# Kernel optimization log

Hardware: AMD Instinct MI355X
Metric: run time of the kernel (lower is better)

Reference implementation:

```python
import jax, jax.numpy as jnp
import numpy as np

C = 512
GROUPS = 8
EPS = 1e-5


def setup_inputs() -> dict:
    key = jax.random.key(0)
    ks = jax.random.split(key, 7)
    B, H, W = 16, 32, 32
    x = jax.random.normal(ks[0], (B, C, H, W), dtype=jnp.float32)
    gamma = jnp.ones((C,), jnp.float32)
    beta = jnp.zeros((C,), jnp.float32)
    # 1x1 convs stored as [out, in] matrices
    w_qkv = jax.random.normal(ks[1], (3 * C, C), dtype=jnp.float32) * (1.0 / np.sqrt(C))
    b_qkv = jax.random.normal(ks[2], (3 * C,), dtype=jnp.float32) * 0.02
    w_proj = jax.random.normal(ks[3], (C, C), dtype=jnp.float32) * (1.0 / np.sqrt(C))
    b_proj = jax.random.normal(ks[4], (C,), dtype=jnp.float32) * 0.02
    return {"x": x, "gamma": gamma, "beta": beta, "w_qkv": w_qkv,
            "b_qkv": b_qkv, "w_proj": w_proj, "b_proj": b_proj}


def _group_norm(x, gamma, beta):
    B, Cc, H, W = x.shape
    xg = x.reshape(B, GROUPS, Cc // GROUPS, H, W)
    mean = xg.mean(axis=(2, 3, 4), keepdims=True)
    var = xg.var(axis=(2, 3, 4), keepdims=True)
    xg = (xg - mean) * jax.lax.rsqrt(var + EPS)
    x = xg.reshape(B, Cc, H, W)
    return x * gamma[None, :, None, None] + beta[None, :, None, None]


def reference(x, gamma, beta, w_qkv, b_qkv, w_proj, b_proj):
    B, Cc, H, W = x.shape
    N = H * W
    h = _group_norm(x, gamma, beta)  # [B,C,H,W]
    hf = h.reshape(B, Cc, N)  # [B,C,N]
    # 1x1 conv == matmul over channel dim
    qkv = jnp.einsum('oc,bcn->bon', w_qkv, hf) + b_qkv[None, :, None]  # [B,3C,N]
    q, k, v = jnp.split(qkv, 3, axis=1)  # each [B,C,N]
    scale = 1.0 / jnp.sqrt(jnp.float32(Cc))
    # attn[b,i,j] = sum_c q[b,c,i] * k[b,c,j]
    attn = jnp.einsum('bci,bcj->bij', q, k) * scale  # [B,N,N]
    attn = jax.nn.softmax(attn, axis=-1)
    out = jnp.einsum('bij,bcj->bci', attn, v)  # [B,C,N]
    out = jnp.einsum('oc,bcn->bon', w_proj, out) + b_proj[None, :, None]
    return x + out.reshape(B, Cc, H, W)
```

## Files before the change

### kernel.cpp

```cpp
#include <hip/hip_runtime.h>
#include <hip/hip_bf16.h>

typedef unsigned short u16;
typedef unsigned int u32;
typedef __attribute__((ext_vector_type(8))) short short8;
typedef __attribute__((ext_vector_type(4))) float floatx4;

#define BATCH 16
#define CDIM 512
#define NSPAT 1024
#define NGROUP 8

__device__ __forceinline__ u16 f2bf(float f) {
    unsigned u = __float_as_uint(f);
    u += 0x7FFFu + ((u >> 16) & 1u);
    return (u16)(u >> 16);
}
__device__ __forceinline__ u32 f2bf2(float lo, float hi) {
    __hip_bfloat162 h = __float22bfloat162_rn(make_float2(lo, hi));
    return *(u32*)&h;
}

__device__ __forceinline__ void load_lds16(const void* g, void* l) {
    __builtin_amdgcn_global_load_lds(
        (const __attribute__((address_space(1))) unsigned int*)g,
        (__attribute__((address_space(3))) unsigned int*)l, 16, 0, 0);
}

#define SBAR0 __builtin_amdgcn_sched_barrier(0)
#define BARRIER { SBAR0; __builtin_amdgcn_s_barrier(); SBAR0; }

__global__ __launch_bounds__(256) void prep_kernel(
    const float* __restrict__ w_qkv, const float* __restrict__ w_proj,
    const float* __restrict__ b_qkv, const float* __restrict__ x,
    u16* __restrict__ wmega, u16* __restrict__ wproj_bf, u16* __restrict__ wv_t,
    float* __restrict__ stats, float* __restrict__ lsums, float* __restrict__ bpv) {
    int b = blockIdx.x;
    int tid = threadIdx.x;
    if (b < 768) {
        const float* src = (b < 512) ? w_qkv : w_proj;
        u16* dst = (b < 512) ? wmega : wproj_bf;
        int i = (b < 512 ? b : b - 512) * 256 + tid;
        float4 v = ((const float4*)src)[i];
        u32* d = (u32*)dst;
        d[i * 2] = f2bf2(v.x, v.y);
        d[i * 2 + 1] = f2bf2(v.z, v.w);
        return;
    }
    if (b < 832) {
        __shared__ u16 t[64 * 66];
        int bt = b - 768;
        int tx = bt & 7, ty = bt >> 3;
        const float* src = w_qkv + (size_t)(1024 + ty * 64) * CDIM + tx * 64;
#pragma unroll
        for (int p = 0; p < 4; ++p) {
            int r = p * 16 + (tid >> 4);
            int c4 = (tid & 15) << 2;
            float4 v = *(const float4*)(src + (size_t)r * CDIM + c4);
            u16* d = &t[r * 66 + c4];
            d[0] = f2bf(v.x); d[1] = f2bf(v.y); d[2] = f2bf(v.z); d[3] = f2bf(v.w);
        }
        __syncthreads();
        u16* dst = wv_t + (size_t)(tx * 64) * CDIM + ty * 64;
#pragma unroll
        for (int p = 0; p < 4; ++p) {
            int c = p * 16 + (tid >> 4);
            int r4 = (tid & 15) << 2;
            ushort4 o;
            o.x = t[(r4 + 0) * 66 + c];
            o.y = t[(r4 + 1) * 66 + c];
            o.z = t[(r4 + 2) * 66 + c];
            o.w = t[(r4 + 3) * 66 + c];
            *(ushort4*)(dst + (size_t)c * CDIM + r4) = o;
        }
        return;
    }
    if (b < 960) {
        __shared__ float rs[4], rss[4];
        int bg = b - 832;
        const float4* xv = (const float4*)(x + (size_t)bg * 65536);
        float s = 0.f, ss = 0.f;
        for (int i = tid; i < 16384; i += 256) {
            float4 v = xv[i];
            s += v.x + v.y + v.z + v.w;
            ss += v.x * v.x + v.y * v.y + v.z * v.z + v.w * v.w;
        }
#pragma unroll
        for (int off = 32; off; off >>= 1) { s += __shfl_down(s, off); ss += __shfl_down(ss, off); }
        int wave = tid >> 6, lane = tid & 63;
        if (lane == 0) { rs[wave] = s; rss[wave] = ss; }
        __syncthreads();
        if (tid == 0) {
            float S1 = rs[0] + rs[1] + rs[2] + rs[3];
            float S2 = rss[0] + rss[1] + rss[2] + rss[3];
            float mean = S1 * (1.f / 65536.f);
            float var = S2 * (1.f / 65536.f) - mean * mean;
            stats[bg * 2] = mean;
            stats[bg * 2 + 1] = rsqrtf(var + 1e-5f);
        }
        return;
    }
    if (b < 976) {
        ((float4*)lsums)[(b - 960) * 256 + tid] = (float4){0.f, 0.f, 0.f, 0.f};
        return;
    }
    {
        int o0 = (b - 976) * 64;
        int wave = tid >> 6, lane = tid & 63;
        const float4* bvv = (const float4*)(b_qkv + 1024);
        float4 v0 = bvv[lane * 2], v1 = bvv[lane * 2 + 1];
        for (int it = 0; it < 16; ++it) {
            int o = o0 + wave * 16 + it;
            const float4* wr = (const float4*)(w_proj + (size_t)o * CDIM);
            float4 a0 = wr[lane * 2], a1 = wr[lane * 2 + 1];
            float s = a0.x * v0.x + a0.y * v0.y + a0.z * v0.z + a0.w * v0.w
                    + a1.x * v1.x + a1.y * v1.y + a1.z * v1.z + a1.w * v1.w;
#pragma unroll
            for (int off = 32; off; off >>= 1) s += __shfl_down(s, off);
            if (lane == 0) bpv[o] = s;
        }
    }
}

__device__ __forceinline__ void stage_tile(
    const u16* __restrict__ Ab, const u16* __restrict__ Bb, int lda, int ldb,
    int m0, int n0, int k0, u16* As, u16* Bs) {
    int tid = threadIdx.x;
#pragma unroll
    for (int it = 0; it < 4; ++it) {
        int c = it * 256 + tid;
        int r = c >> 3, p = c & 7;
        int kc = p ^ (r & 7);
        load_lds16(Ab + (size_t)(m0 + r) * lda + k0 + (kc << 3), &As[c << 3]);
        load_lds16(Bb + (size_t)(n0 + r) * ldb + k0 + (kc << 3), &Bs[c << 3]);
    }
}

__device__ __forceinline__ void compute_tile(
    const u16* As, const u16* Bs, int wm, int wn, int quad, int lrow,
    floatx4 (&acc)[4][4]) {
#pragma unroll
    for (int s = 0; s < 2; ++s) {
        short8 af[4], bf[4];
#pragma unroll
        for (int i = 0; i < 4; ++i) {
            int R = wm + i * 16 + lrow;
            int p = (s * 4 + quad) ^ (R & 7);
            af[i] = *(const short8*)&As[(R << 6) + (p << 3)];
        }
#pragma unroll
        for (int j = 0; j < 4; ++j) {
            int R = wn + j * 16 + lrow;
            int p = (s * 4 + quad) ^ (R & 7);
            bf[j] = *(const short8*)&Bs[(R << 6) + (p << 3)];
        }
#pragma unroll
        for (int i = 0; i < 4; ++i)
#pragma unroll
            for (int j = 0; j < 4; ++j)
                acc[i][j] = __builtin_amdgcn_mfma_f32_16x16x32_bf16(af[i], bf[j], acc[i][j], 0, 0, 0);
    }
}

__device__ __forceinline__ void gemm_core_sb(
    const u16* __restrict__ Ab, const u16* __restrict__ Bb, int K, int lda, int ldb,
    int m0, int n0, u16* As, u16* Bs, floatx4 (&acc)[4][4]) {
    int tid = threadIdx.x;
    int lane = tid & 63, wave = tid >> 6, quad = lane >> 4, lrow = lane & 15;
    int wm = (wave >> 1) << 6, wn = (wave & 1) << 6;
    for (int k0 = 0; k0 < K; k0 += 64) {
        stage_tile(Ab, Bb, lda, ldb, m0, n0, k0, As, Bs);
        __syncthreads();
        compute_tile(As, Bs, wm, wn, quad, lrow, acc);
        __syncthreads();
    }
}

#define ACC_INIT floatx4 acc[4][4]; \
    _Pragma("unroll") for (int i = 0; i < 4; ++i) \
    _Pragma("unroll") for (int j = 0; j < 4; ++j) acc[i][j] = (floatx4){0.f, 0.f, 0.f, 0.f};

#define EPILOG_IDX int lane = threadIdx.x & 63, wave = threadIdx.x >> 6; \
    int quad = lane >> 4, lrow = lane & 15; \
    int wm = (wave >> 1) << 6, wn = (wave & 1) << 6;

__device__ __forceinline__ void issueA2(
    const u16* __restrict__ Ab, int lda, int m0, int t, int h, u16* smem) {
    int tid = threadIdx.x;
    u16* base = smem + (t & 1) * 16384 + h * 8192;
#pragma unroll
    for (int l = 0; l < 2; ++l) {
        int c = l * 512 + tid;
        int rho = c >> 3, p = c & 7;
        int kc = p ^ (rho & 7);
        int r = ((rho >> 6) << 7) | (h << 6) | (rho & 63);
        load_lds16(Ab + (size_t)(m0 + r) * lda + (t << 6) + (kc << 3), base + (c << 3));
    }
}
__device__ __forceinline__ void issueB2(
    const u16* __restrict__ Bb, int ldb, int n0, int t, int h, u16* smem) {
    int tid = threadIdx.x;
    u16* base = smem + 32768 + (t & 1) * 16384 + h * 8192;
#pragma unroll
    for (int l = 0; l < 2; ++l) {
        int c = l * 512 + tid;
        int rho = c >> 3, p = c & 7;
        int kc = p ^ (rho & 7);
        int r = ((rho >> 5) << 6) | (h << 5) | (rho & 31);
        load_lds16(Bb + (size_t)(n0 + r) * ldb + (t << 6) + (kc << 3), base + (c << 3));
    }
}

__device__ __forceinline__ void gemm256x256(
    const u16* __restrict__ Ab, const u16* __restrict__ Bb, int K, int lda, int ldb,
    int m0, int n0, u16* smem, floatx4 (&acc)[8][4]) {
    int tid = threadIdx.x;
    int lane = tid & 63, wave = tid >> 6;
    int quad = lane >> 4, lrow = lane & 15;
    int wrow = wave >> 2, wcol = wave & 3;
    int nt = K >> 6;
    issueA2(Ab, lda, m0, 0, 0, smem);
    issueA2(Ab, lda, m0, 0, 1, smem);
    issueB2(Bb, ldb, n0, 0, 0, smem);
    issueB2(Bb, ldb, n0, 0, 1, smem);
    for (int t = 0; t < nt; ++t) {
        int slot = t & 1;
        BARRIER;
        if (t + 1 < nt) {
            issueA2(Ab, lda, m0, t + 1, 0, smem);
            issueA2(Ab, lda, m0, t + 1, 1, smem);
            issueB2(Bb, ldb, n0, t + 1, 0, smem);
            issueB2(Bb, ldb, n0, t + 1, 1, smem);
            asm volatile("s_waitcnt vmcnt(8)" ::: "memory");
        } else {
            asm volatile("s_waitcnt vmcnt(0)" ::: "memory");
        }
        BARRIER;
        const u16* Ah = smem + slot * 16384;
        const u16* Bh = smem + 32768 + slot * 16384;
        short8 bf[2][4];
#pragma unroll
        for (int qn = 0; qn < 2; ++qn)
#pragma unroll
            for (int ks = 0; ks < 2; ++ks)
#pragma unroll
                for (int j = 0; j < 2; ++j) {
                    int rho = wcol * 32 + j * 16 + lrow;
                    int p = (ks * 4 + quad) ^ (lrow & 7);
                    bf[qn][ks * 2 + j] = *(const short8*)&Bh[qn * 8192 + (rho << 6) + (p << 3)];
                }
#pragma unroll
        for (int qm = 0; qm < 2; ++qm) {
            short8 af[8];
#pragma unroll
            for (int ks = 0; ks < 2; ++ks)
#pragma unroll
                for (int i = 0; i < 4; ++i) {
                    int rho = wrow * 64 + i * 16 + lrow;
                    int p = (ks * 4 + quad) ^ (lrow & 7);
                    af[ks * 4 + i] = *(const short8*)&Ah[qm * 8192 + (rho << 6) + (p << 3)];
                }
#pragma unroll
            for (int ks = 0; ks < 2; ++ks)
#pragma unroll
                for (int i = 0; i < 4; ++i)
#pragma unroll
                    for (int qn = 0; qn < 2; ++qn)
#pragma unroll
                        for (int j = 0; j < 2; ++j)
                            acc[qm * 4 + i][qn * 2 + j] = __builtin_amdgcn_mfma_f32_16x16x32_bf16(
                                af[ks * 4 + i], bf[qn][ks * 2 + j], acc[qm * 4 + i][qn * 2 + j], 0, 0, 0);
        }
    }
}

__device__ __forceinline__ void issueA4(
    const u16* __restrict__ Ab, int lda, int m0, int t, u16* smem) {
    int tid = threadIdx.x;
    u16* base = smem + (t & 1) * 16384;
#pragma unroll
    for (int l = 0; l < 4; ++l) {
        int c = l * 512 + tid;
        int rho = c >> 3, p = c & 7;
        int kc = p ^ (rho & 7);
        load_lds16(Ab + (size_t)(m0 + rho) * lda + (t << 6) + (kc << 3), base + (c << 3));
    }
}
__device__ __forceinline__ void issueB4(
    const u16* __restrict__ Bb, int ldb, int n0, int t, int h, u16* smem) {
    int tid = threadIdx.x;
    u16* base = smem + 32768 + (t & 1) * 8192 + h * 4096;
    int rho = tid >> 3, p = tid & 7;
    int kc = p ^ (rho & 7);
    int r = ((rho >> 5) << 6) | (h << 5) | (rho & 31);
    load_lds16(Bb + (size_t)(n0 + r) * ldb + (t << 6) + (kc << 3), base + (tid << 3));
}

__device__ __forceinline__ void gemm256x128(
    const u16* __restrict__ Ab, const u16* __restrict__ Bb, int K, int lda, int ldb,
    int m0, int n0, u16* smem, floatx4 (&acc)[4][4]) {
    int tid = threadIdx.x;
    int lane = tid & 63, wave = tid >> 6;
    int quad = lane >> 4, lrow = lane & 15;
    int wrow = wave >> 1, wcol = wave & 1;
    int nt = K >> 6;
    issueA4(Ab, lda, m0, 0, smem);
    issueB4(Bb, ldb, n0, 0, 0, smem);
    issueB4(Bb, ldb, n0, 0, 1, smem);
    for (int t = 0; t < nt; ++t) {
        int slot = t & 1;
        BARRIER;
        if (t + 1 < nt) {
            issueA4(Ab, lda, m0, t + 1, smem);
            issueB4(Bb, ldb, n0, t + 1, 0, smem);
            issueB4(Bb, ldb, n0, t + 1, 1, smem);
            asm volatile("s_waitcnt vmcnt(6)" ::: "memory");
        } else {
            asm volatile("s_waitcnt vmcnt(0)" ::: "memory");
        }
        BARRIER;
        const u16* Ah = smem + slot * 16384;
        const u16* Bh = smem + 32768 + slot * 8192;
        short8 bf[2][4];
#pragma unroll
        for (int qn = 0; qn < 2; ++qn)
#pragma unroll
            for (int ks = 0; ks < 2; ++ks)
#pragma unroll
                for (int j = 0; j < 2; ++j) {
                    int rho = wcol * 32 + j * 16 + lrow;
                    int p = (ks * 4 + quad) ^ (lrow & 7);
                    bf[qn][ks * 2 + j] = *(const short8*)&Bh[qn * 4096 + (rho << 6) + (p << 3)];
                }
        short8 af[8];
#pragma unroll
        for (int ks = 0; ks < 2; ++ks)
#pragma unroll
            for (int i = 0; i < 4; ++i) {
                int rho = wrow * 64 + i * 16 + lrow;
                int p = (ks * 4 + quad) ^ (lrow & 7);
                af[ks * 4 + i] = *(const short8*)&Ah[(rho << 6) + (p << 3)];
            }
#pragma unroll
        for (int ks = 0; ks < 2; ++ks)
#pragma unroll
            for (int i = 0; i < 4; ++i)
#pragma unroll
                for (int qn = 0; qn < 2; ++qn)
#pragma unroll
                    for (int j = 0; j < 2; ++j)
                        acc[i][qn * 2 + j] = __builtin_amdgcn_mfma_f32_16x16x32_bf16(
                            af[ks * 4 + i], bf[qn][ks * 2 + j], acc[i][qn * 2 + j], 0, 0, 0);
    }
}

#define ACC_INIT84 floatx4 acc[8][4]; \
    _Pragma("unroll") for (int i = 0; i < 8; ++i) \
    _Pragma("unroll") for (int j = 0; j < 4; ++j) acc[i][j] = (floatx4){0.f, 0.f, 0.f, 0.f};

#define ACC_INIT44 floatx4 acc[4][4]; \
    _Pragma("unroll") for (int i = 0; i < 4; ++i) \
    _Pragma("unroll") for (int j = 0; j < 4; ++j) acc[i][j] = (floatx4){0.f, 0.f, 0.f, 0.f};

#define TSTR 66
__global__ __launch_bounds__(256) void gn_wpv_kernel(
    const float* __restrict__ x, const float* __restrict__ gamma, const float* __restrict__ beta,
    const float* __restrict__ stats, u16* __restrict__ hT,
    const u16* __restrict__ wproj_bf, const u16* __restrict__ wv_t, u16* __restrict__ wmega) {
    __shared__ u16 smem[2 * 128 * 64];
    int tid = threadIdx.x;
    if (blockIdx.z == 16) {
        if (blockIdx.x >= 4 || blockIdx.y >= 4) return;
        int m0 = blockIdx.y << 7, n0 = blockIdx.x << 7;
        ACC_INIT;
        gemm_core_sb(wproj_bf, wv_t, CDIM, CDIM, CDIM, m0, n0, smem, smem + 128 * 64, acc);
        EPILOG_IDX;
#pragma unroll
        for (int i = 0; i < 4; ++i)
#pragma unroll
            for (int j = 0; j < 4; ++j)
#pragma unroll
                for (int r = 0; r < 4; ++r) {
                    int R = m0 + wm + i * 16 + (quad << 2) + r;
                    int Cc = n0 + wn + j * 16 + lrow;
                    wmega[(size_t)(1024 + R) * CDIM + Cc] = f2bf(acc[i][j][r]);
                }
        return;
    }
    u16* t = smem;
    int b = blockIdx.z, c0 = blockIdx.y << 6, n0 = blockIdx.x << 6;
    const float* xb = x + ((size_t)b * CDIM + c0) * NSPAT + n0;
#pragma unroll
    for (int p = 0; p < 4; ++p) {
        int cl = p * 16 + (tid >> 4);
        int nl = (tid & 15) << 2;
        int c = c0 + cl;
        int bg = b * NGROUP + (c >> 6);
        float ga = gamma[c] * stats[bg * 2 + 1];
        float be = beta[c] - stats[bg * 2] * ga;
        float4 v = *(const float4*)(xb + (size_t)cl * NSPAT + nl);
        u16* dst = &t[cl * TSTR + nl];
        dst[0] = f2bf(v.x * ga + be);
        dst[1] = f2bf(v.y * ga + be);
        dst[2] = f2bf(v.z * ga + be);
        dst[3] = f2bf(v.w * ga + be);
    }
    __syncthreads();
    u16* hb = hT + ((size_t)b * NSPAT + n0) * CDIM + c0;
#pragma unroll
    for (int p = 0; p < 4; ++p) {
        int nl = p * 16 + (tid >> 4);
        int cl4 = (tid & 15) << 2;
        ushort4 o;
        o.x = t[(cl4 + 0) * TSTR + nl];
        o.y = t[(cl4 + 1) * TSTR + nl];
        o.z = t[(cl4 + 2) * TSTR + nl];
        o.w = t[(cl4 + 3) * TSTR + nl];
        *(ushort4*)(hb + (size_t)nl * CDIM + cl4) = o;
    }
}

__global__ __launch_bounds__(512, 2) void qkv_kernel(
    const u16* __restrict__ wmega, const u16* __restrict__ hT,
    const float* __restrict__ b_qkv, const float* __restrict__ bpv,
    u16* __restrict__ qkT, u16* __restrict__ WV) {
    extern __shared__ u16 smem[];
    int z = blockIdx.x;
    int n0 = blockIdx.y << 8;
    int m0 = blockIdx.z << 8;
    const u16* Bb = hT + (size_t)z * CDIM * NSPAT;
    ACC_INIT84;
    gemm256x256(wmega, Bb, CDIM, CDIM, CDIM, m0, n0, smem, acc);
    int lane = threadIdx.x & 63, wave = threadIdx.x >> 6;
    int quad = lane >> 4, lrow = lane & 15;
    int wrow = wave >> 2, wcol = wave & 3;
    if (blockIdx.z < 4) {
        u16* qk = qkT + (size_t)z * NSPAT * NSPAT;
#pragma unroll
        for (int mf = 0; mf < 8; ++mf) {
            int R0 = m0 + wrow * 128 + mf * 16 + (quad << 2);
            float4 bv = *(const float4*)&b_qkv[R0];
#pragma unroll
            for (int nf = 0; nf < 4; ++nf) {
                int Cc = n0 + wcol * 64 + nf * 16 + lrow;
                uint2 u;
                u.x = f2bf2(acc[mf][nf][0] + bv.x, acc[mf][nf][1] + bv.y);
                u.y = f2bf2(acc[mf][nf][2] + bv.z, acc[mf][nf][3] + bv.w);
                *(uint2*)&qk[(size_t)Cc * NSPAT + R0] = u;
            }
        }
    } else {
        u16* Wp = WV + (size_t)z * CDIM * NSPAT;
#pragma unroll
        for (int mf = 0; mf < 8; ++mf) {
            int R = m0 - 1024 + wrow * 128 + mf * 16 + (quad << 2);
            float4 pv = *(const float4*)&bpv[R];
#pragma unroll
            for (int nf = 0; nf < 4; ++nf) {
                int Cc = n0 + wcol * 64 + nf * 16 + lrow;
                Wp[(size_t)(R + 0) * NSPAT + Cc] = f2bf(acc[mf][nf][0] + pv.x);
                Wp[(size_t)(R + 1) * NSPAT + Cc] = f2bf(acc[mf][nf][1] + pv.y);
                Wp[(size_t)(R + 2) * NSPAT + Cc] = f2bf(acc[mf][nf][2] + pv.z);
                Wp[(size_t)(R + 3) * NSPAT + Cc] = f2bf(acc[mf][nf][3] + pv.w);
            }
        }
    }
}

__global__ __launch_bounds__(512, 2) void scores_kernel(
    const u16* __restrict__ qkT, u16* __restrict__ P, float* __restrict__ lsums, float scale) {
    extern __shared__ u16 smem[];
    int z = blockIdx.x;
    int n0 = blockIdx.y << 8;
    int m0 = blockIdx.z << 8;
    const u16* qb = qkT + (size_t)z * NSPAT * NSPAT;
    ACC_INIT84;
    gemm256x256(qb + CDIM, qb, CDIM, NSPAT, NSPAT, m0, n0, smem, acc);
    int lane = threadIdx.x & 63, wave = threadIdx.x >> 6;
    int quad = lane >> 4, lrow = lane & 15;
    int wrow = wave >> 2, wcol = wave & 3;
    u16* Pp = P + (size_t)z * NSPAT * NSPAT;
    float* ls = lsums + (size_t)z * NSPAT;
#pragma unroll
    for (int nf = 0; nf < 4; ++nf) {
        int Ci = n0 + wcol * 64 + nf * 16 + lrow;
        float part = 0.f;
#pragma unroll
        for (int mf = 0; mf < 8; ++mf) {
            int Rj0 = m0 + wrow * 128 + mf * 16 + (quad << 2);
            float e0 = __expf(acc[mf][nf][0] * scale);
            float e1 = __expf(acc[mf][nf][1] * scale);
            float e2 = __expf(acc[mf][nf][2] * scale);
            float e3 = __expf(acc[mf][nf][3] * scale);
            part += (e0 + e1) + (e2 + e3);
            uint2 u;
            u.x = f2bf2(e0, e1);
            u.y = f2bf2(e2, e3);
            *(uint2*)&Pp[(size_t)Ci * NSPAT + Rj0] = u;
        }
        part += __shfl_xor(part, 16);
        part += __shfl_xor(part, 32);
        if (lane < 16) atomicAdd(&ls[Ci], part);
    }
}

__global__ __launch_bounds__(512, 2) void final_kernel(
    const u16* __restrict__ WV, const u16* __restrict__ P, const float* __restrict__ lsums,
    const float* __restrict__ bias, const float* __restrict__ x, float* __restrict__ out) {
    extern __shared__ u16 smem[];
    int z = blockIdx.x;
    int n0 = blockIdx.y << 7;
    int m0 = blockIdx.z << 8;
    const u16* Pb = P + (size_t)z * NSPAT * NSPAT;
    const u16* WVb = WV + (size_t)z * CDIM * NSPAT;
    ACC_INIT44;
    gemm256x128(Pb, WVb, NSPAT, NSPAT, NSPAT, m0, n0, smem, acc);
    int lane = threadIdx.x & 63, wave = threadIdx.x >> 6;
    int quad = lane >> 4, lrow = lane & 15;
    int wrow = wave >> 1, wcol = wave & 1;
    float* Op = out + (size_t)z * CDIM * NSPAT;
    const float* xr = x + (size_t)z * CDIM * NSPAT;
    const float* li = lsums + (size_t)z * NSPAT;
#pragma unroll
    for (int mf = 0; mf < 4; ++mf) {
        int Ri0 = m0 + wrow * 64 + mf * 16 + (quad << 2);
        float4 lv = *(const float4*)&li[Ri0];
        float s0 = __builtin_amdgcn_rcpf(lv.x);
        float s1 = __builtin_amdgcn_rcpf(lv.y);
        float s2 = __builtin_amdgcn_rcpf(lv.z);
        float s3 = __builtin_amdgcn_rcpf(lv.w);
#pragma unroll
        for (int nf = 0; nf < 4; ++nf) {
            int Co = n0 + wcol * 64 + nf * 16 + lrow;
            float bv = bias[Co];
            size_t off = (size_t)Co * NSPAT + Ri0;
            float4 xv = *(const float4*)&xr[off];
            float4 o;
            o.x = acc[mf][nf][0] * s0 + bv + xv.x;
            o.y = acc[mf][nf][1] * s1 + bv + xv.y;
            o.z = acc[mf][nf][2] * s2 + bv + xv.z;
            o.w = acc[mf][nf][3] * s3 + bv + xv.w;
            *(float4*)&Op[off] = o;
        }
    }
}

extern "C" void kernel_launch(void* const* d_in, const int* in_sizes, int n_in,
                              void* d_out, int out_size, void* d_ws, size_t ws_size,
                              hipStream_t stream) {
    const float* x      = (const float*)d_in[0];
    const float* gamma  = (const float*)d_in[1];
    const float* beta   = (const float*)d_in[2];
    const float* w_qkv  = (const float*)d_in[3];
    const float* b_qkv  = (const float*)d_in[4];
    const float* w_proj = (const float*)d_in[5];
    const float* b_proj = (const float*)d_in[6];
    float* out = (float*)d_out;

    const size_t CN = (size_t)CDIM * NSPAT;
    const size_t NN = (size_t)NSPAT * NSPAT;
    const float SCALE = 0.044194173824159216f;
    const int LDS_BIG = 131072;
    const int LDS_MED = 98304;

    static bool lds_attr_done = false;
    if (!lds_attr_done) {
        hipFuncSetAttribute((const void*)qkv_kernel,
                            hipFuncAttributeMaxDynamicSharedMemorySize, LDS_BIG);
        hipFuncSetAttribute((const void*)scores_kernel,
                            hipFuncAttributeMaxDynamicSharedMemorySize, LDS_BIG);
        hipFuncSetAttribute((const void*)final_kernel,
                            hipFuncAttributeMaxDynamicSharedMemorySize, LDS_MED);
        lds_attr_done = true;
    }

    char* ws = (char*)d_ws;
    float* stats   = (float*)ws;
    float* bpv     = (float*)(ws + 1024);
    u16* wmega     = (u16*)(ws + 4096);
    u16* wproj_bf  = wmega + (size_t)3 * CDIM * CDIM;
    u16* wv_t      = wproj_bf + (size_t)CDIM * CDIM;
    u16* hT        = wv_t + (size_t)CDIM * CDIM;
    u16* qkT       = hT + BATCH * CN;
    u16* WV        = qkT + BATCH * NN;
    u16* P         = WV + BATCH * CN;
    float* lsums   = (float*)(P + BATCH * NN);

    prep_kernel<<<984, 256, 0, stream>>>(
        w_qkv, w_proj, b_qkv, x, wmega, wproj_bf, wv_t, stats, lsums, bpv);

    gn_wpv_kernel<<<dim3(16, 8, 17), 256, 0, stream>>>(
        x, gamma, beta, stats, hT, wproj_bf, wv_t, wmega);

    qkv_kernel<<<dim3(BATCH, 4, 6), 512, LDS_BIG, stream>>>(
        wmega, hT, b_qkv, bpv, qkT, WV);

    scores_kernel<<<dim3(BATCH, 4, 4), 512, LDS_BIG, stream>>>(qkT, P, lsums, SCALE);

    final_kernel<<<dim3(BATCH, 4, 4), 512, LDS_MED, stream>>>(WV, P, lsums, b_proj, x, out);
}
```

Baseline: 134.8 us.

## Switch GEMMs to 256x128 tiles with triple-buffered LDS prefetch

```diff
diff --git a/kernel.cpp b/kernel.cpp
--- a/kernel.cpp
+++ b/kernel.cpp
@@ -184,100 +184,14 @@
     int quad = lane >> 4, lrow = lane & 15; \
     int wm = (wave >> 1) << 6, wn = (wave & 1) << 6;
 
-__device__ __forceinline__ void issueA2(
-    const u16* __restrict__ Ab, int lda, int m0, int t, int h, u16* smem) {
-    int tid = threadIdx.x;
-    u16* base = smem + (t & 1) * 16384 + h * 8192;
-#pragma unroll
-    for (int l = 0; l < 2; ++l) {
-        int c = l * 512 + tid;
-        int rho = c >> 3, p = c & 7;
-        int kc = p ^ (rho & 7);
-        int r = ((rho >> 6) << 7) | (h << 6) | (rho & 63);
-        load_lds16(Ab + (size_t)(m0 + r) * lda + (t << 6) + (kc << 3), base + (c << 3));
-    }
-}
-__device__ __forceinline__ void issueB2(
-    const u16* __restrict__ Bb, int ldb, int n0, int t, int h, u16* smem) {
-    int tid = threadIdx.x;
-    u16* base = smem + 32768 + (t & 1) * 16384 + h * 8192;
-#pragma unroll
-    for (int l = 0; l < 2; ++l) {
-        int c = l * 512 + tid;
-        int rho = c >> 3, p = c & 7;
-        int kc = p ^ (rho & 7);
-        int r = ((rho >> 5) << 6) | (h << 5) | (rho & 31);
-        load_lds16(Bb + (size_t)(n0 + r) * ldb + (t << 6) + (kc << 3), base + (c << 3));
-    }
-}
-
-__device__ __forceinline__ void gemm256x256(
-    const u16* __restrict__ Ab, const u16* __restrict__ Bb, int K, int lda, int ldb,
-    int m0, int n0, u16* smem, floatx4 (&acc)[8][4]) {
-    int tid = threadIdx.x;
-    int lane = tid & 63, wave = tid >> 6;
-    int quad = lane >> 4, lrow = lane & 15;
-    int wrow = wave >> 2, wcol = wave & 3;
-    int nt = K >> 6;
-    issueA2(Ab, lda, m0, 0, 0, smem);
-    issueA2(Ab, lda, m0, 0, 1, smem);
-    issueB2(Bb, ldb, n0, 0, 0, smem);
-    issueB2(Bb, ldb, n0, 0, 1, smem);
-    for (int t = 0; t < nt; ++t) {
-        int slot = t & 1;
-        BARRIER;
-        if (t + 1 < nt) {
-            issueA2(Ab, lda, m0, t + 1, 0, smem);
-            issueA2(Ab, lda, m0, t + 1, 1, smem);
-            issueB2(Bb, ldb, n0, t + 1, 0, smem);
-            issueB2(Bb, ldb, n0, t + 1, 1, smem);
-            asm volatile("s_waitcnt vmcnt(8)" ::: "memory");
-        } else {
-            asm volatile("s_waitcnt vmcnt(0)" ::: "memory");
-        }
-        BARRIER;
-        const u16* Ah = smem + slot * 16384;
-        const u16* Bh = smem + 32768 + slot * 16384;
-        short8 bf[2][4];
-#pragma unroll
-        for (int qn = 0; qn < 2; ++qn)
-#pragma unroll
-            for (int ks = 0; ks < 2; ++ks)
-#pragma unroll
-                for (int j = 0; j < 2; ++j) {
-                    int rho = wcol * 32 + j * 16 + lrow;
-                    int p = (ks * 4 + quad) ^ (lrow & 7);
-                    bf[qn][ks * 2 + j] = *(const short8*)&Bh[qn * 8192 + (rho << 6) + (p << 3)];
-                }
-#pragma unroll
-        for (int qm = 0; qm < 2; ++qm) {
-            short8 af[8];
-#pragma unroll
-            for (int ks = 0; ks < 2; ++ks)
-#pragma unroll
-                for (int i = 0; i < 4; ++i) {
-                    int rho = wrow * 64 + i * 16 + lrow;
-                    int p = (ks * 4 + quad) ^ (lrow & 7);
-                    af[ks * 4 + i] = *(const short8*)&Ah[qm * 8192 + (rho << 6) + (p << 3)];
-                }
-#pragma unroll
-            for (int ks = 0; ks < 2; ++ks)
-#pragma unroll
-                for (int i = 0; i < 4; ++i)
-#pragma unroll
-                    for (int qn = 0; qn < 2; ++qn)
-#pragma unroll
-                        for (int j = 0; j < 2; ++j)
-                            acc[qm * 4 + i][qn * 2 + j] = __builtin_amdgcn_mfma_f32_16x16x32_bf16(
-                                af[ks * 4 + i], bf[qn][ks * 2 + j], acc[qm * 4 + i][qn * 2 + j], 0, 0, 0);
-        }
-    }
-}
-
-__device__ __forceinline__ void issueA4(
-    const u16* __restrict__ Ab, int lda, int m0, int t, u16* smem) {
-    int tid = threadIdx.x;
-    u16* base = smem + (t & 1) * 16384;
+#define ASLOT 16384
+#define BSLOT 8192
+#define BBASE 49152
+
+__device__ __forceinline__ void issueA3(
+    const u16* __restrict__ Ab, int lda, int m0, int t, int slot, u16* smem) {
+    int tid = threadIdx.x;
+    u16* base = smem + slot * ASLOT;
 #pragma unroll
     for (int l = 0; l < 4; ++l) {
         int c = l * 512 + tid;
@@ -286,17 +200,20 @@
         load_lds16(Ab + (size_t)(m0 + rho) * lda + (t << 6) + (kc << 3), base + (c << 3));
     }
 }
-__device__ __forceinline__ void issueB4(
-    const u16* __restrict__ Bb, int ldb, int n0, int t, int h, u16* smem) {
-    int tid = threadIdx.x;
-    u16* base = smem + 32768 + (t & 1) * 8192 + h * 4096;
-    int rho = tid >> 3, p = tid & 7;
-    int kc = p ^ (rho & 7);
-    int r = ((rho >> 5) << 6) | (h << 5) | (rho & 31);
-    load_lds16(Bb + (size_t)(n0 + r) * ldb + (t << 6) + (kc << 3), base + (tid << 3));
-}
-
-__device__ __forceinline__ void gemm256x128(
+__device__ __forceinline__ void issueB3(
+    const u16* __restrict__ Bb, int ldb, int n0, int t, int slot, u16* smem) {
+    int tid = threadIdx.x;
+    u16* base = smem + BBASE + slot * BSLOT;
+#pragma unroll
+    for (int l = 0; l < 2; ++l) {
+        int c = l * 512 + tid;
+        int rho = c >> 3, p = c & 7;
+        int kc = p ^ (rho & 7);
+        load_lds16(Bb + (size_t)(n0 + rho) * ldb + (t << 6) + (kc << 3), base + (c << 3));
+    }
+}
+
+__device__ __forceinline__ void gemm256x128_3s(
     const u16* __restrict__ Ab, const u16* __restrict__ Bb, int K, int lda, int ldb,
     int m0, int n0, u16* smem, floatx4 (&acc)[4][4]) {
     int tid = threadIdx.x;
@@ -304,34 +221,34 @@
     int quad = lane >> 4, lrow = lane & 15;
     int wrow = wave >> 1, wcol = wave & 1;
     int nt = K >> 6;
-    issueA4(Ab, lda, m0, 0, smem);
-    issueB4(Bb, ldb, n0, 0, 0, smem);
-    issueB4(Bb, ldb, n0, 0, 1, smem);
+    issueA3(Ab, lda, m0, 0, 0, smem);
+    issueB3(Bb, ldb, n0, 0, 0, smem);
+    issueA3(Ab, lda, m0, 1, 1, smem);
+    issueB3(Bb, ldb, n0, 1, 1, smem);
+    int slot = 0, slot2 = 2;
     for (int t = 0; t < nt; ++t) {
-        int slot = t & 1;
         BARRIER;
-        if (t + 1 < nt) {
-            issueA4(Ab, lda, m0, t + 1, smem);
-            issueB4(Bb, ldb, n0, t + 1, 0, smem);
-            issueB4(Bb, ldb, n0, t + 1, 1, smem);
+        if (t + 2 < nt) {
+            issueA3(Ab, lda, m0, t + 2, slot2, smem);
+            issueB3(Bb, ldb, n0, t + 2, slot2, smem);
+            asm volatile("s_waitcnt vmcnt(12)" ::: "memory");
+        } else if (t + 1 < nt) {
             asm volatile("s_waitcnt vmcnt(6)" ::: "memory");
         } else {
             asm volatile("s_waitcnt vmcnt(0)" ::: "memory");
         }
         BARRIER;
-        const u16* Ah = smem + slot * 16384;
-        const u16* Bh = smem + 32768 + slot * 8192;
-        short8 bf[2][4];
-#pragma unroll
-        for (int qn = 0; qn < 2; ++qn)
-#pragma unroll
-            for (int ks = 0; ks < 2; ++ks)
-#pragma unroll
-                for (int j = 0; j < 2; ++j) {
-                    int rho = wcol * 32 + j * 16 + lrow;
-                    int p = (ks * 4 + quad) ^ (lrow & 7);
-                    bf[qn][ks * 2 + j] = *(const short8*)&Bh[qn * 4096 + (rho << 6) + (p << 3)];
-                }
+        const u16* Ah = smem + slot * ASLOT;
+        const u16* Bh = smem + BBASE + slot * BSLOT;
+        short8 bf[8];
+#pragma unroll
+        for (int ks = 0; ks < 2; ++ks)
+#pragma unroll
+            for (int j = 0; j < 4; ++j) {
+                int rho = wcol * 64 + j * 16 + lrow;
+                int p = (ks * 4 + quad) ^ (lrow & 7);
+                bf[ks * 4 + j] = *(const short8*)&Bh[(rho << 6) + (p << 3)];
+            }
         short8 af[8];
 #pragma unroll
         for (int ks = 0; ks < 2; ++ks)
@@ -346,21 +263,21 @@
 #pragma unroll
             for (int i = 0; i < 4; ++i)
 #pragma unroll
-                for (int qn = 0; qn < 2; ++qn)
-#pragma unroll
-                    for (int j = 0; j < 2; ++j)
-                        acc[i][qn * 2 + j] = __builtin_amdgcn_mfma_f32_16x16x32_bf16(
-                            af[ks * 4 + i], bf[qn][ks * 2 + j], acc[i][qn * 2 + j], 0, 0, 0);
-    }
-}
-
-#define ACC_INIT84 floatx4 acc[8][4]; \
-    _Pragma("unroll") for (int i = 0; i < 8; ++i) \
-    _Pragma("unroll") for (int j = 0; j < 4; ++j) acc[i][j] = (floatx4){0.f, 0.f, 0.f, 0.f};
+                for (int j = 0; j < 4; ++j)
+                    acc[i][j] = __builtin_amdgcn_mfma_f32_16x16x32_bf16(
+                        af[ks * 4 + i], bf[ks * 4 + j], acc[i][j], 0, 0, 0);
+        slot = (slot == 2) ? 0 : slot + 1;
+        slot2 = (slot2 == 2) ? 0 : slot2 + 1;
+    }
+}
 
 #define ACC_INIT44 floatx4 acc[4][4]; \
     _Pragma("unroll") for (int i = 0; i < 4; ++i) \
     _Pragma("unroll") for (int j = 0; j < 4; ++j) acc[i][j] = (floatx4){0.f, 0.f, 0.f, 0.f};
+
+#define EPILOG_IDX8 int lane = threadIdx.x & 63, wave = threadIdx.x >> 6; \
+    int quad = lane >> 4, lrow = lane & 15; \
+    int wrow = wave >> 1, wcol = wave & 1;
 
 #define TSTR 66
 __global__ __launch_bounds__(256) void gn_wpv_kernel(
@@ -420,25 +337,23 @@
     }
 }
 
-__global__ __launch_bounds__(512, 2) void qkv_kernel(
+__global__ __launch_bounds__(512, 1) void qkv_kernel(
     const u16* __restrict__ wmega, const u16* __restrict__ hT,
     const float* __restrict__ b_qkv, const float* __restrict__ bpv,
     u16* __restrict__ qkT, u16* __restrict__ WV) {
     extern __shared__ u16 smem[];
     int z = blockIdx.x;
-    int n0 = blockIdx.y << 8;
+    int n0 = blockIdx.y << 7;
     int m0 = blockIdx.z << 8;
     const u16* Bb = hT + (size_t)z * CDIM * NSPAT;
-    ACC_INIT84;
-    gemm256x256(wmega, Bb, CDIM, CDIM, CDIM, m0, n0, smem, acc);
-    int lane = threadIdx.x & 63, wave = threadIdx.x >> 6;
-    int quad = lane >> 4, lrow = lane & 15;
-    int wrow = wave >> 2, wcol = wave & 3;
+    ACC_INIT44;
+    gemm256x128_3s(wmega, Bb, CDIM, CDIM, CDIM, m0, n0, smem, acc);
+    EPILOG_IDX8;
     if (blockIdx.z < 4) {
         u16* qk = qkT + (size_t)z * NSPAT * NSPAT;
 #pragma unroll
-        for (int mf = 0; mf < 8; ++mf) {
-            int R0 = m0 + wrow * 128 + mf * 16 + (quad << 2);
+        for (int mf = 0; mf < 4; ++mf) {
+            int R0 = m0 + wrow * 64 + mf * 16 + (quad << 2);
             float4 bv = *(const float4*)&b_qkv[R0];
 #pragma unroll
             for (int nf = 0; nf < 4; ++nf) {
@@ -452,8 +367,8 @@
     } else {
         u16* Wp = WV + (size_t)z * CDIM * NSPAT;
 #pragma unroll
-        for (int mf = 0; mf < 8; ++mf) {
-            int R = m0 - 1024 + wrow * 128 + mf * 16 + (quad << 2);
+        for (int mf = 0; mf < 4; ++mf) {
+            int R = m0 - 1024 + wrow * 64 + mf * 16 + (quad << 2);
             float4 pv = *(const float4*)&bpv[R];
 #pragma unroll
             for (int nf = 0; nf < 4; ++nf) {
@@ -467,18 +382,16 @@
     }
 }
 
-__global__ __launch_bounds__(512, 2) void scores_kernel(
+__global__ __launch_bounds__(512, 1) void scores_kernel(
     const u16* __restrict__ qkT, u16* __restrict__ P, float* __restrict__ lsums, float scale) {
     extern __shared__ u16 smem[];
     int z = blockIdx.x;
-    int n0 = blockIdx.y << 8;
+    int n0 = blockIdx.y << 7;
     int m0 = blockIdx.z << 8;
     const u16* qb = qkT + (size_t)z * NSPAT * NSPAT;
-    ACC_INIT84;
-    gemm256x256(qb + CDIM, qb, CDIM, NSPAT, NSPAT, m0, n0, smem, acc);
-    int lane = threadIdx.x & 63, wave = threadIdx.x >> 6;
-    int quad = lane >> 4, lrow = lane & 15;
-    int wrow = wave >> 2, wcol = wave & 3;
+    ACC_INIT44;
+    gemm256x128_3s(qb + CDIM, qb, CDIM, NSPAT, NSPAT, m0, n0, smem, acc);
+    EPILOG_IDX8;
     u16* Pp = P + (size_t)z * NSPAT * NSPAT;
     float* ls = lsums + (size_t)z * NSPAT;
 #pragma unroll
@@ -486,8 +399,8 @@
         int Ci = n0 + wcol * 64 + nf * 16 + lrow;
         float part = 0.f;
 #pragma unroll
-        for (int mf = 0; mf < 8; ++mf) {
-            int Rj0 = m0 + wrow * 128 + mf * 16 + (quad << 2);
+        for (int mf = 0; mf < 4; ++mf) {
+            int Rj0 = m0 + wrow * 64 + mf * 16 + (quad << 2);
             float e0 = __expf(acc[mf][nf][0] * scale);
             float e1 = __expf(acc[mf][nf][1] * scale);
             float e2 = __expf(acc[mf][nf][2] * scale);
@@ -504,7 +417,7 @@
     }
 }
 
-__global__ __launch_bounds__(512, 2) void final_kernel(
+__global__ __launch_bounds__(512, 1) void final_kernel(
     const u16* __restrict__ WV, const u16* __restrict__ P, const float* __restrict__ lsums,
     const float* __restrict__ bias, const float* __restrict__ x, float* __restrict__ out) {
     extern __shared__ u16 smem[];
@@ -514,10 +427,8 @@
     const u16* Pb = P + (size_t)z * NSPAT * NSPAT;
     const u16* WVb = WV + (size_t)z * CDIM * NSPAT;
     ACC_INIT44;
-    gemm256x128(Pb, WVb, NSPAT, NSPAT, NSPAT, m0, n0, smem, acc);
-    int lane = threadIdx.x & 63, wave = threadIdx.x >> 6;
-    int quad = lane >> 4, lrow = lane & 15;
-    int wrow = wave >> 1, wcol = wave & 1;
+    gemm256x128_3s(Pb, WVb, NSPAT, NSPAT, NSPAT, m0, n0, smem, acc);
+    EPILOG_IDX8;
     float* Op = out + (size_t)z * CDIM * NSPAT;
     const float* xr = x + (size_t)z * CDIM * NSPAT;
     const float* li = lsums + (size_t)z * NSPAT;
@@ -560,17 +471,16 @@
     const size_t CN = (size_t)CDIM * NSPAT;
     const size_t NN = (size_t)NSPAT * NSPAT;
     const float SCALE = 0.044194173824159216f;
-    const int LDS_BIG = 131072;
-    const int LDS_MED = 98304;
+    const int LDS_3S = (3 * (ASLOT + BSLOT)) * 2;
 
     static bool lds_attr_done = false;
     if (!lds_attr_done) {
         hipFuncSetAttribute((const void*)qkv_kernel,
-                            hipFuncAttributeMaxDynamicSharedMemorySize, LDS_BIG);
+                            hipFuncAttributeMaxDynamicSharedMemorySize, LDS_3S);
         hipFuncSetAttribute((const void*)scores_kernel,
-                            hipFuncAttributeMaxDynamicSharedMemorySize, LDS_BIG);
+                            hipFuncAttributeMaxDynamicSharedMemorySize, LDS_3S);
         hipFuncSetAttribute((const void*)final_kernel,
-                            hipFuncAttributeMaxDynamicSharedMemorySize, LDS_MED);
+                            hipFuncAttributeMaxDynamicSharedMemorySize, LDS_3S);
         lds_attr_done = true;
     }
 
@@ -592,10 +502,10 @@
     gn_wpv_kernel<<<dim3(16, 8, 17), 256, 0, stream>>>(
         x, gamma, beta, stats, hT, wproj_bf, wv_t, wmega);
 
-    qkv_kernel<<<dim3(BATCH, 4, 6), 512, LDS_BIG, stream>>>(
+    qkv_kernel<<<dim3(BATCH, 8, 6), 512, LDS_3S, stream>>>(
         wmega, hT, b_qkv, bpv, qkT, WV);
 
-    scores_kernel<<<dim3(BATCH, 4, 4), 512, LDS_BIG, stream>>>(qkT, P, lsums, SCALE);
-
-    final_kernel<<<dim3(BATCH, 4, 4), 512, LDS_MED, stream>>>(WV, P, lsums, b_proj, x, out);
-}
+    scores_kernel<<<dim3(BATCH, 8, 4), 512, LDS_3S, stream>>>(qkT, P, lsums, SCALE);
+
+    final_kernel<<<dim3(BATCH, 4, 4), 512, LDS_3S, stream>>>(WV, P, lsums, b_proj, x, out);
+}
```

Result: slower. 140.9 us (+4.6%).

## Fold Wq^T Wk into a single precomputed matrix to shrink the QK projection

Applied to the files above, without the earlier changes.

```diff
diff --git a/kernel.cpp b/kernel.cpp
--- a/kernel.cpp
+++ b/kernel.cpp
@@ -20,6 +20,10 @@
     __hip_bfloat162 h = __float22bfloat162_rn(make_float2(lo, hi));
     return *(u32*)&h;
 }
+__device__ __forceinline__ float bf2f(u16 v) {
+    u32 t = ((u32)v) << 16;
+    return __uint_as_float(t);
+}
 
 __device__ __forceinline__ void load_lds16(const void* g, void* l) {
     __builtin_amdgcn_global_load_lds(
@@ -33,25 +37,27 @@
 __global__ __launch_bounds__(256) void prep_kernel(
     const float* __restrict__ w_qkv, const float* __restrict__ w_proj,
     const float* __restrict__ b_qkv, const float* __restrict__ x,
-    u16* __restrict__ wmega, u16* __restrict__ wproj_bf, u16* __restrict__ wv_t,
-    float* __restrict__ stats, float* __restrict__ lsums, float* __restrict__ bpv) {
+    u16* __restrict__ wproj_bf, u16* __restrict__ wq_t, u16* __restrict__ wk_t,
+    u16* __restrict__ wv_t, float* __restrict__ stats, float* __restrict__ lsums,
+    float* __restrict__ bpv, float* __restrict__ cvec) {
     int b = blockIdx.x;
     int tid = threadIdx.x;
-    if (b < 768) {
-        const float* src = (b < 512) ? w_qkv : w_proj;
-        u16* dst = (b < 512) ? wmega : wproj_bf;
-        int i = (b < 512 ? b : b - 512) * 256 + tid;
-        float4 v = ((const float4*)src)[i];
-        u32* d = (u32*)dst;
+    if (b < 256) {
+        int i = b * 256 + tid;
+        float4 v = ((const float4*)w_proj)[i];
+        u32* d = (u32*)wproj_bf;
         d[i * 2] = f2bf2(v.x, v.y);
         d[i * 2 + 1] = f2bf2(v.z, v.w);
         return;
     }
-    if (b < 832) {
+    if (b < 448) {
         __shared__ u16 t[64 * 66];
-        int bt = b - 768;
-        int tx = bt & 7, ty = bt >> 3;
-        const float* src = w_qkv + (size_t)(1024 + ty * 64) * CDIM + tx * 64;
+        int bt = b - 256;
+        int which = bt >> 6;
+        int bt2 = bt & 63;
+        int tx = bt2 & 7, ty = bt2 >> 3;
+        const float* src = w_qkv + (size_t)(which * 512 + ty * 64) * CDIM + tx * 64;
+        u16* dstb = (which == 0) ? wq_t : (which == 1) ? wk_t : wv_t;
 #pragma unroll
         for (int p = 0; p < 4; ++p) {
             int r = p * 16 + (tid >> 4);
@@ -61,7 +67,7 @@
             d[0] = f2bf(v.x); d[1] = f2bf(v.y); d[2] = f2bf(v.z); d[3] = f2bf(v.w);
         }
         __syncthreads();
-        u16* dst = wv_t + (size_t)(tx * 64) * CDIM + ty * 64;
+        u16* dst = dstb + (size_t)(tx * 64) * CDIM + ty * 64;
 #pragma unroll
         for (int p = 0; p < 4; ++p) {
             int c = p * 16 + (tid >> 4);
@@ -75,9 +81,9 @@
         }
         return;
     }
-    if (b < 960) {
+    if (b < 576) {
         __shared__ float rs[4], rss[4];
-        int bg = b - 832;
+        int bg = b - 448;
         const float4* xv = (const float4*)(x + (size_t)bg * 65536);
         float s = 0.f, ss = 0.f;
         for (int i = tid; i < 16384; i += 256) {
@@ -100,12 +106,12 @@
         }
         return;
     }
-    if (b < 976) {
-        ((float4*)lsums)[(b - 960) * 256 + tid] = (float4){0.f, 0.f, 0.f, 0.f};
+    if (b < 592) {
+        ((float4*)lsums)[(b - 576) * 256 + tid] = (float4){0.f, 0.f, 0.f, 0.f};
         return;
     }
-    {
-        int o0 = (b - 976) * 64;
+    if (b < 600) {
+        int o0 = (b - 592) * 64;
         int wave = tid >> 6, lane = tid & 63;
         const float4* bvv = (const float4*)(b_qkv + 1024);
         float4 v0 = bvv[lane * 2], v1 = bvv[lane * 2 + 1];
@@ -119,6 +125,14 @@
             for (int off = 32; off; off >>= 1) s += __shfl_down(s, off);
             if (lane == 0) bpv[o] = s;
         }
+        return;
+    }
+    {
+        int col = (b - 600) * 256 + tid;
+        float s = 0.f;
+        for (int m = 0; m < 512; ++m)
+            s += w_qkv[(size_t)(512 + m) * CDIM + col] * b_qkv[m];
+        cvec[col] = s;
     }
 }
 
@@ -366,14 +380,20 @@
 __global__ __launch_bounds__(256) void gn_wpv_kernel(
     const float* __restrict__ x, const float* __restrict__ gamma, const float* __restrict__ beta,
     const float* __restrict__ stats, u16* __restrict__ hT,
-    const u16* __restrict__ wproj_bf, const u16* __restrict__ wv_t, u16* __restrict__ wmega) {
+    const u16* __restrict__ wproj_bf, const u16* __restrict__ wq_t,
+    const u16* __restrict__ wk_t, const u16* __restrict__ wv_t, u16* __restrict__ wmega) {
     __shared__ u16 smem[2 * 128 * 64];
     int tid = threadIdx.x;
     if (blockIdx.z == 16) {
-        if (blockIdx.x >= 4 || blockIdx.y >= 4) return;
-        int m0 = blockIdx.y << 7, n0 = blockIdx.x << 7;
+        if (blockIdx.x >= 4) return;
+        bool isM = blockIdx.y < 4;
+        int m0 = (isM ? blockIdx.y : blockIdx.y - 4) << 7;
+        int n0 = blockIdx.x << 7;
+        const u16* Aop = isM ? wq_t : wproj_bf;
+        const u16* Bop = isM ? wk_t : wv_t;
+        int rbase = isM ? 0 : 512;
         ACC_INIT;
-        gemm_core_sb(wproj_bf, wv_t, CDIM, CDIM, CDIM, m0, n0, smem, smem + 128 * 64, acc);
+        gemm_core_sb(Aop, Bop, CDIM, CDIM, CDIM, m0, n0, smem, smem + 128 * 64, acc);
         EPILOG_IDX;
 #pragma unroll
         for (int i = 0; i < 4; ++i)
@@ -383,7 +403,7 @@
                 for (int r = 0; r < 4; ++r) {
                     int R = m0 + wm + i * 16 + (quad << 2) + r;
                     int Cc = n0 + wn + j * 16 + lrow;
-                    wmega[(size_t)(1024 + R) * CDIM + Cc] = f2bf(acc[i][j][r]);
+                    wmega[(size_t)(rbase + R) * CDIM + Cc] = f2bf(acc[i][j][r]);
                 }
         return;
     }
@@ -422,10 +442,33 @@
 
 __global__ __launch_bounds__(512, 2) void qkv_kernel(
     const u16* __restrict__ wmega, const u16* __restrict__ hT,
-    const float* __restrict__ b_qkv, const float* __restrict__ bpv,
-    u16* __restrict__ qkT, u16* __restrict__ WV) {
+    const float* __restrict__ cvec, const float* __restrict__ bpv,
+    u16* __restrict__ gT, u16* __restrict__ WV, float* __restrict__ rbuf) {
     extern __shared__ u16 smem[];
     int z = blockIdx.x;
+    if (blockIdx.y == 4) {
+        if (blockIdx.z != 0) return;
+        int tid = threadIdx.x;
+        const u16* hb = hT + (size_t)z * CDIM * NSPAT;
+#pragma unroll 1
+        for (int jj = 0; jj < 2; ++jj) {
+            int j = tid * 2 + jj;
+            const short8* hp = (const short8*)(hb + (size_t)j * CDIM);
+            float s = 0.f;
+#pragma unroll 4
+            for (int cc = 0; cc < 64; ++cc) {
+                short8 v = hp[cc];
+                const float4* cv = (const float4*)&cvec[cc * 8];
+                float4 c0 = cv[0], c1 = cv[1];
+                s += c0.x * bf2f((u16)v[0]) + c0.y * bf2f((u16)v[1])
+                   + c0.z * bf2f((u16)v[2]) + c0.w * bf2f((u16)v[3])
+                   + c1.x * bf2f((u16)v[4]) + c1.y * bf2f((u16)v[5])
+                   + c1.z * bf2f((u16)v[6]) + c1.w * bf2f((u16)v[7]);
+            }
+            rbuf[(size_t)z * NSPAT + j] = s;
+        }
+        return;
+    }
     int n0 = blockIdx.y << 8;
     int m0 = blockIdx.z << 8;
     const u16* Bb = hT + (size_t)z * CDIM * NSPAT;
@@ -434,26 +477,25 @@
     int lane = threadIdx.x & 63, wave = threadIdx.x >> 6;
     int quad = lane >> 4, lrow = lane & 15;
     int wrow = wave >> 2, wcol = wave & 3;
-    if (blockIdx.z < 4) {
-        u16* qk = qkT + (size_t)z * NSPAT * NSPAT;
+    if (blockIdx.z < 2) {
+        u16* gp = gT + (size_t)z * NSPAT * CDIM;
 #pragma unroll
         for (int mf = 0; mf < 8; ++mf) {
             int R0 = m0 + wrow * 128 + mf * 16 + (quad << 2);
-            float4 bv = *(const float4*)&b_qkv[R0];
 #pragma unroll
             for (int nf = 0; nf < 4; ++nf) {
                 int Cc = n0 + wcol * 64 + nf * 16 + lrow;
                 uint2 u;
-                u.x = f2bf2(acc[mf][nf][0] + bv.x, acc[mf][nf][1] + bv.y);
-                u.y = f2bf2(acc[mf][nf][2] + bv.z, acc[mf][nf][3] + bv.w);
-                *(uint2*)&qk[(size_t)Cc * NSPAT + R0] = u;
+                u.x = f2bf2(acc[mf][nf][0], acc[mf][nf][1]);
+                u.y = f2bf2(acc[mf][nf][2], acc[mf][nf][3]);
+                *(uint2*)&gp[(size_t)Cc * CDIM + R0] = u;
             }
         }
     } else {
         u16* Wp = WV + (size_t)z * CDIM * NSPAT;
 #pragma unroll
         for (int mf = 0; mf < 8; ++mf) {
-            int R = m0 - 1024 + wrow * 128 + mf * 16 + (quad << 2);
+            int R = m0 - 512 + wrow * 128 + mf * 16 + (quad << 2);
             float4 pv = *(const float4*)&bpv[R];
 #pragma unroll
             for (int nf = 0; nf < 4; ++nf) {
@@ -468,19 +510,23 @@
 }
 
 __global__ __launch_bounds__(512, 2) void scores_kernel(
-    const u16* __restrict__ qkT, u16* __restrict__ P, float* __restrict__ lsums, float scale) {
+    const u16* __restrict__ gT, const u16* __restrict__ hT,
+    u16* __restrict__ P, float* __restrict__ lsums, const float* __restrict__ rbuf,
+    float scale) {
     extern __shared__ u16 smem[];
     int z = blockIdx.x;
     int n0 = blockIdx.y << 8;
     int m0 = blockIdx.z << 8;
-    const u16* qb = qkT + (size_t)z * NSPAT * NSPAT;
+    const u16* gb = gT + (size_t)z * NSPAT * CDIM;
+    const u16* hb = hT + (size_t)z * CDIM * NSPAT;
     ACC_INIT84;
-    gemm256x256(qb + CDIM, qb, CDIM, NSPAT, NSPAT, m0, n0, smem, acc);
+    gemm256x256(gb, hb, CDIM, CDIM, CDIM, m0, n0, smem, acc);
     int lane = threadIdx.x & 63, wave = threadIdx.x >> 6;
     int quad = lane >> 4, lrow = lane & 15;
     int wrow = wave >> 2, wcol = wave & 3;
     u16* Pp = P + (size_t)z * NSPAT * NSPAT;
     float* ls = lsums + (size_t)z * NSPAT;
+    const float* rb = rbuf + (size_t)z * NSPAT;
 #pragma unroll
     for (int nf = 0; nf < 4; ++nf) {
         int Ci = n0 + wcol * 64 + nf * 16 + lrow;
@@ -488,10 +534,11 @@
 #pragma unroll
         for (int mf = 0; mf < 8; ++mf) {
             int Rj0 = m0 + wrow * 128 + mf * 16 + (quad << 2);
-            float e0 = __expf(acc[mf][nf][0] * scale);
-            float e1 = __expf(acc[mf][nf][1] * scale);
-            float e2 = __expf(acc[mf][nf][2] * scale);
-            float e3 = __expf(acc[mf][nf][3] * scale);
+            float4 rv = *(const float4*)&rb[Rj0];
+            float e0 = __expf((acc[mf][nf][0] + rv.x) * scale);
+            float e1 = __expf((acc[mf][nf][1] + rv.y) * scale);
+            float e2 = __expf((acc[mf][nf][2] + rv.z) * scale);
+            float e3 = __expf((acc[mf][nf][3] + rv.w) * scale);
             part += (e0 + e1) + (e2 + e3);
             uint2 u;
             u.x = f2bf2(e0, e1);
@@ -577,25 +624,30 @@
     char* ws = (char*)d_ws;
     float* stats   = (float*)ws;
     float* bpv     = (float*)(ws + 1024);
-    u16* wmega     = (u16*)(ws + 4096);
-    u16* wproj_bf  = wmega + (size_t)3 * CDIM * CDIM;
-    u16* wv_t      = wproj_bf + (size_t)CDIM * CDIM;
+    float* cvec    = (float*)(ws + 3072);
+    u16* wmega     = (u16*)(ws + 8192);
+    u16* wproj_bf  = wmega + (size_t)1024 * CDIM;
+    u16* wq_t      = wproj_bf + (size_t)CDIM * CDIM;
+    u16* wk_t      = wq_t + (size_t)CDIM * CDIM;
+    u16* wv_t      = wk_t + (size_t)CDIM * CDIM;
     u16* hT        = wv_t + (size_t)CDIM * CDIM;
-    u16* qkT       = hT + BATCH * CN;
-    u16* WV        = qkT + BATCH * NN;
+    u16* gT        = hT + BATCH * CN;
+    u16* WV        = gT + BATCH * CN;
     u16* P         = WV + BATCH * CN;
     float* lsums   = (float*)(P + BATCH * NN);
-
-    prep_kernel<<<984, 256, 0, stream>>>(
-        w_qkv, w_proj, b_qkv, x, wmega, wproj_bf, wv_t, stats, lsums, bpv);
+    float* rbuf    = lsums + (size_t)BATCH * NSPAT;
+
+    prep_kernel<<<602, 256, 0, stream>>>(
+        w_qkv, w_proj, b_qkv, x, wproj_bf, wq_t, wk_t, wv_t, stats, lsums, bpv, cvec);
 
     gn_wpv_kernel<<<dim3(16, 8, 17), 256, 0, stream>>>(
-        x, gamma, beta, stats, hT, wproj_bf, wv_t, wmega);
-
-    qkv_kernel<<<dim3(BATCH, 4, 6), 512, LDS_BIG, stream>>>(
-        wmega, hT, b_qkv, bpv, qkT, WV);
-
-    scores_kernel<<<dim3(BATCH, 4, 4), 512, LDS_BIG, stream>>>(qkT, P, lsums, SCALE);
+        x, gamma, beta, stats, hT, wproj_bf, wq_t, wk_t, wv_t, wmega);
+
+    qkv_kernel<<<dim3(BATCH, 5, 4), 512, LDS_BIG, stream>>>(
+        wmega, hT, cvec, bpv, gT, WV, rbuf);
+
+    scores_kernel<<<dim3(BATCH, 4, 4), 512, LDS_BIG, stream>>>(
+        gT, hT, P, lsums, rbuf, SCALE);
 
     final_kernel<<<dim3(BATCH, 4, 4), 512, LDS_MED, stream>>>(WV, P, lsums, b_proj, x, out);
 }
```

Result: no change. 136.6 us (+1.4%).
